# Kernel optimization log

Hardware: AMD Instinct MI355X
Metric: run time of the kernel (lower is better)

Reference implementation:

```python
import jax, jax.numpy as jnp
import numpy as np

NUM_NODES = 10000  # fixed by input spec: edge_index values in [0, 10000)


def setup_inputs() -> dict:
    key = jax.random.key(0)
    k1, k2, k3 = jax.random.split(key, 3)
    N, E, D_IN, D_OUT = NUM_NODES, 320000, 256, 256
    x = jax.random.normal(k1, (N, D_IN), dtype=jnp.float32)
    edge_index = jax.random.randint(k2, (2, E), 0, N, dtype=jnp.int64)
    # ensure node N-1 appears so num_nodes == N as in the torch code
    edge_index = edge_index.at[0, 0].set(N - 1)
    # xavier_uniform for [D_IN, D_OUT]
    limit = float(np.sqrt(6.0 / (D_IN + D_OUT)))
    weight = jax.random.uniform(k3, (D_IN, D_OUT), dtype=jnp.float32,
                                minval=-limit, maxval=limit)
    return {"x": x, "edge_index": edge_index, "weight": weight}


def _normalize_adjacency(edge_index, num_nodes):
    src, dst = edge_index[0], edge_index[1]
    ones = jnp.ones(src.shape[0], dtype=jnp.float32)
    # symmetric binarized adjacency: adj[i,j] = adj[j,i] = 1 (set, not add)
    adj = jnp.zeros((num_nodes, num_nodes), dtype=jnp.float32)
    adj = adj.at[src, dst].max(ones)
    adj = adj.at[dst, src].max(ones)
    # one round of self-loops: adj += I
    adj = adj + jnp.eye(num_nodes, dtype=jnp.float32)
    deg = jnp.sum(adj, axis=1)                    # [N]
    dinv = 1.0 / jnp.sqrt(deg)                    # [N]
    # D^-1/2 A D^-1/2 via broadcasting (equivalent to diag mms)
    return adj * dinv[:, None] * dinv[None, :]


def reference(x, edge_index, weight):
    adj = _normalize_adjacency(edge_index, NUM_NODES)  # [N, N]
    h = adj @ x                                        # [N, D_IN]
    return h @ weight                                  # [N, D_OUT]
```

## Files before the change

### kernel.cpp

```cpp
#include <hip/hip_runtime.h>
#include <hip/hip_bf16.h>
#include <stdint.h>

#define N_NODES   10000
#define D_FEAT    256
#define E_EDGES   320000
#define ROW_WORDS 313
#define ROW_STRIDE 320
#define LIST_CAP  1024

#define NB     250
#define RPB    40
#define B_CAP  8192
#define NBLK_E 313
#define NBLK_W 64
#define RPC    20

#define LDSTR 264

typedef __attribute__((ext_vector_type(4))) float float4v;
typedef _Float16 half8  __attribute__((ext_vector_type(8)));
typedef _Float16 half4v __attribute__((ext_vector_type(4)));

__device__ __forceinline__ uint16_t f2bf(float f) {
    union { float f; uint32_t u; } v; v.f = f;
    uint32_t r = v.u + 0x7fffu + ((v.u >> 16) & 1u);
    return (uint16_t)(r >> 16);
}
__device__ __forceinline__ float lo16(uint32_t u) {
    union { uint32_t u; float f; } v; v.u = u << 16; return v.f;
}
__device__ __forceinline__ float hi16(uint32_t u) {
    union { uint32_t u; float f; } v; v.u = u & 0xffff0000u; return v.f;
}


__global__ void __launch_bounds__(1024)
fill_buckets(const int* __restrict__ ei, uint32_t* __restrict__ bucketbuf,
             uint32_t* __restrict__ cursors,
             const float* __restrict__ w, _Float16* __restrict__ wt) {
    __shared__ uint32_t hist[256];
    __shared__ uint32_t lofs[256];
    __shared__ uint32_t base_s[256];
    __shared__ uint32_t stage[2048];
    __shared__ uint16_t sbkt[2048];
    int t = threadIdx.x;

    if (blockIdx.x >= NBLK_E) {
        int kb = (blockIdx.x - NBLK_E) * 4;
        int k = kb + (t >> 8), n = t & 255;
        float* st = (float*)stage;
        st[(n << 2) | (t >> 8)] = w[(size_t)k * D_FEAT + n];
        __syncthreads();
        if (t < 256) {
            half4v o = { (_Float16)st[t * 4 + 0], (_Float16)st[t * 4 + 1],
                         (_Float16)st[t * 4 + 2], (_Float16)st[t * 4 + 3] };
            *(half4v*)&wt[(size_t)t * D_FEAT + kb] = o;
        }
        return;
    }

    if (t < 256) hist[t] = 0;
    __syncthreads();
    int e = blockIdx.x * 1024 + t;
    int b0 = -1, b1 = -1; uint32_t ent0 = 0, ent1 = 0, s0 = 0, s1 = 0;
    if (e < E_EDGES) {
        int s = ei[e], d = ei[E_EDGES + e];
        if ((uint32_t)s < N_NODES && (uint32_t)d < N_NODES) {
            b0 = s / RPB; ent0 = ((uint32_t)(s - b0 * RPB) << 14) | (uint32_t)d;
            b1 = d / RPB; ent1 = ((uint32_t)(d - b1 * RPB) << 14) | (uint32_t)s;
            s0 = atomicAdd(&hist[b0], 1u);
            s1 = atomicAdd(&hist[b1], 1u);
        }
    }
    __syncthreads();
    if (t < 256) lofs[t] = hist[t];
    __syncthreads();
    for (int d = 1; d < 256; d <<= 1) {
        uint32_t v = 0;
        if (t < 256 && t >= d) v = lofs[t - d];
        __syncthreads();
        if (t < 256) lofs[t] += v;
        __syncthreads();
    }
    if (t < 256) base_s[t] = hist[t] ? atomicAdd(&cursors[t], hist[t]) : 0u;
    if (b0 >= 0) {
        uint32_t p0 = lofs[b0] - hist[b0] + s0;
        stage[p0] = ent0; sbkt[p0] = (uint16_t)b0;
        uint32_t p1 = lofs[b1] - hist[b1] + s1;
        stage[p1] = ent1; sbkt[p1] = (uint16_t)b1;
    }
    __syncthreads();
    uint32_t total = lofs[255];
    for (uint32_t idx = t; idx < total; idx += 1024) {
        uint32_t b = sbkt[idx];
        uint32_t pos = base_s[b] + (idx - (lofs[b] - hist[b]));
        if (pos < B_CAP) bucketbuf[(size_t)b * B_CAP + pos] = stage[idx];
    }
}

__global__ void __launch_bounds__(1024)
bucket_to_csr(const uint32_t* __restrict__ bucketbuf,
              const uint32_t* __restrict__ cursors,
              uint32_t* __restrict__ gcursor,
              uint32_t* __restrict__ col, uint32_t* __restrict__ row_base,
              uint32_t* __restrict__ row_deg, float* __restrict__ dinv,
              const float* __restrict__ x, uint16_t* __restrict__ xs) {
    __shared__ uint32_t bm[RPC * ROW_WORDS];
    __shared__ uint32_t degs[RPC];
    __shared__ uint32_t rowoff[RPC];
    __shared__ uint32_t segbase;
    int blk = blockIdx.x, t = threadIdx.x;
    int b   = blk >> 1;
    int lr0 = (blk & 1) * RPC;
    for (int i = t; i < RPC * ROW_WORDS; i += 1024) bm[i] = 0;
    __syncthreads();
    uint32_t cnt = min(cursors[b], (uint32_t)B_CAP);
    const uint32_t* bb = bucketbuf + (size_t)b * B_CAP;
    for (uint32_t i = t; i < cnt; i += 1024) {
        uint32_t ent = bb[i];
        uint32_t lr = (ent >> 14) - (uint32_t)lr0;
        if (lr < RPC) {
            uint32_t d = ent & 0x3FFFu;
            atomicOr(&bm[lr * ROW_WORDS + (d >> 5)], 1u << (d & 31));
        }
    }
    __syncthreads();
    int wv = t >> 6, lane = t & 63;
    for (int r = wv; r < RPC; r += 16) {
        int pop = 0;
        #pragma unroll
        for (int k = 0; k < 5; k++) {
            int w = lane + 64 * k;
            if (w < ROW_WORDS) pop += __popc(bm[r * ROW_WORDS + w]);
        }
        #pragma unroll
        for (int off = 32; off > 0; off >>= 1) pop += __shfl_xor(pop, off, 64);
        if (lane == 0) degs[r] = (uint32_t)pop;
    }
    __syncthreads();
    if (t == 0) {
        uint32_t run = 0;
        for (int r = 0; r < RPC; r++) {
            rowoff[r] = run;
            run += (degs[r] + 3u) & ~3u;
        }
        segbase = atomicAdd(gcursor, run);
    }
    __syncthreads();
    int row0 = b * RPB + lr0;
    for (int r = wv; r < RPC; r += 16) {
        int gi = row0 + r;
        uint32_t base = segbase + rowoff[r];
        float di = 1.0f / sqrtf((float)(degs[r] + 1u));
        if (lane == 0) {
            row_base[gi] = base;
            row_deg[gi]  = degs[r];
            dinv[gi]     = di;
        }
        float4v xv = *(const float4v*)(x + (size_t)gi * D_FEAT + lane * 4);
        uint2 o;
        o.x = (uint32_t)f2bf(di * xv[0]) | ((uint32_t)f2bf(di * xv[1]) << 16);
        o.y = (uint32_t)f2bf(di * xv[2]) | ((uint32_t)f2bf(di * xv[3]) << 16);
        *(uint2*)(xs + (size_t)gi * D_FEAT + lane * 4) = o;
        uint32_t wb[5]; int tot = 0;
        #pragma unroll
        for (int k = 0; k < 5; k++) {
            int w = lane + 64 * k;
            uint32_t v = (w < ROW_WORDS) ? bm[r * ROW_WORDS + w] : 0u;
            wb[k] = v; tot += __popc(v);
        }
        int incl = tot;
        #pragma unroll
        for (int off = 1; off < 64; off <<= 1) {
            int v = __shfl_up(incl, off, 64);
            if (lane >= off) incl += v;
        }
        uint32_t p = base + (uint32_t)(incl - tot);
        #pragma unroll
        for (int k = 0; k < 5; k++) {
            uint32_t bits = wb[k];
            uint32_t cbase = (uint32_t)(lane + 64 * k) << 5;
            while (bits) {
                col[p++] = cbase + (uint32_t)__builtin_ctz(bits);
                bits &= bits - 1;
            }
        }
    }
}

__global__ void __launch_bounds__(256)
spmm_csr(const uint32_t* __restrict__ row_base, const uint32_t* __restrict__ row_deg,
         const float* __restrict__ dinv, const uint32_t* __restrict__ col,
         const uint16_t* __restrict__ xs, _Float16* __restrict__ aggh) {
    int wv = threadIdx.x >> 6, lane = threadIdx.x & 63;
    int i = blockIdx.x * 4 + wv;
    uint32_t base = row_base[i], deg = row_deg[i];
    float di = dinv[i];
    float4v z = {0.f, 0.f, 0.f, 0.f};
    float4v a0 = z, a1 = z, a2 = z, a3 = z, a4 = z, a5 = z, a6 = z, a7 = z;
    size_t ch = (size_t)lane * 4;
    uint32_t t8 = deg & ~7u;
    uint32_t t = 0;
    for (; t < t8; t += 8) {
        uint4 jva = *(const uint4*)&col[base + t];
        uint4 jvb = *(const uint4*)&col[base + t + 4];
        uint2 g0 = *(const uint2*)(xs + (size_t)jva.x * D_FEAT + ch);
        uint2 g1 = *(const uint2*)(xs + (size_t)jva.y * D_FEAT + ch);
        uint2 g2 = *(const uint2*)(xs + (size_t)jva.z * D_FEAT + ch);
        uint2 g3 = *(const uint2*)(xs + (size_t)jva.w * D_FEAT + ch);
        uint2 g4 = *(const uint2*)(xs + (size_t)jvb.x * D_FEAT + ch);
        uint2 g5 = *(const uint2*)(xs + (size_t)jvb.y * D_FEAT + ch);
        uint2 g6 = *(const uint2*)(xs + (size_t)jvb.z * D_FEAT + ch);
        uint2 g7 = *(const uint2*)(xs + (size_t)jvb.w * D_FEAT + ch);
        a0[0] += lo16(g0.x); a0[1] += hi16(g0.x); a0[2] += lo16(g0.y); a0[3] += hi16(g0.y);
        a1[0] += lo16(g1.x); a1[1] += hi16(g1.x); a1[2] += lo16(g1.y); a1[3] += hi16(g1.y);
        a2[0] += lo16(g2.x); a2[1] += hi16(g2.x); a2[2] += lo16(g2.y); a2[3] += hi16(g2.y);
        a3[0] += lo16(g3.x); a3[1] += hi16(g3.x); a3[2] += lo16(g3.y); a3[3] += hi16(g3.y);
        a4[0] += lo16(g4.x); a4[1] += hi16(g4.x); a4[2] += lo16(g4.y); a4[3] += hi16(g4.y);
        a5[0] += lo16(g5.x); a5[1] += hi16(g5.x); a5[2] += lo16(g5.y); a5[3] += hi16(g5.y);
        a6[0] += lo16(g6.x); a6[1] += hi16(g6.x); a6[2] += lo16(g6.y); a6[3] += hi16(g6.y);
        a7[0] += lo16(g7.x); a7[1] += hi16(g7.x); a7[2] += lo16(g7.y); a7[3] += hi16(g7.y);
    }
    for (; t < deg; t++) {
        uint32_t j = col[base + t];
        uint2 g = *(const uint2*)(xs + (size_t)j * D_FEAT + ch);
        a0[0] += lo16(g.x); a0[1] += hi16(g.x); a0[2] += lo16(g.y); a0[3] += hi16(g.y);
    }
    uint2 gs = *(const uint2*)(xs + (size_t)i * D_FEAT + ch);
    a1[0] += lo16(gs.x); a1[1] += hi16(gs.x); a1[2] += lo16(gs.y); a1[3] += hi16(gs.y);
    float4v acc = ((a0 + a1) + (a2 + a3)) + ((a4 + a5) + (a6 + a7));
    half4v o = { (_Float16)(di * acc[0]), (_Float16)(di * acc[1]),
                 (_Float16)(di * acc[2]), (_Float16)(di * acc[3]) };
    *(half4v*)(aggh + (size_t)i * D_FEAT + ch) = o;
}

__global__ void __launch_bounds__(256)
gemm_mfma(const _Float16* __restrict__ aggh, const _Float16* __restrict__ wt,
          float* __restrict__ out) {
    __shared__ __align__(16) _Float16 a_lds[16 * LDSTR];
    int t = threadIdx.x, wv = t >> 6, lane = t & 63;
    int r0 = blockIdx.x * 16;
    for (int idx = t * 8; idx < 16 * D_FEAT; idx += 256 * 8) {
        int r = idx >> 8, c = idx & 255;
        *(half8*)&a_lds[r * LDSTR + c] =
            *(const half8*)&aggh[(size_t)(r0 + r) * D_FEAT + c];
    }
    __syncthreads();
    int quad = lane >> 4, r = lane & 15;
    int mbase = r0 + quad * 4;
    #pragma unroll
    for (int u = 0; u < 4; u++) {
        int ct = wv * 4 + u;
        const _Float16* pb = wt + (size_t)(ct * 16 + r) * D_FEAT + quad * 8;
        float4v acc = {0.f, 0.f, 0.f, 0.f};
        #pragma unroll
        for (int kk = 0; kk < D_FEAT; kk += 32) {
            half8 a = *(const half8*)&a_lds[r * LDSTR + kk + quad * 8];
            half8 b = *(const half8*)(pb + kk);
            acc = __builtin_amdgcn_mfma_f32_16x16x32_f16(a, b, acc, 0, 0, 0);
        }
        int colg = ct * 16 + r;
        #pragma unroll
        for (int v = 0; v < 4; v++)
            out[(size_t)(mbase + v) * D_FEAT + colg] = acc[v];
    }
}


__global__ void scatter_edges_fb(const int* __restrict__ ei,
                                 uint32_t* __restrict__ bitmap) {
    int e = blockIdx.x * blockDim.x + threadIdx.x;
    if (e >= E_EDGES) return;
    int s = ei[e], d = ei[E_EDGES + e];
    if ((uint32_t)s >= N_NODES || (uint32_t)d >= N_NODES) return;
    atomicOr(&bitmap[(size_t)s * ROW_STRIDE + (d >> 5)], 1u << (d & 31));
    atomicOr(&bitmap[(size_t)d * ROW_STRIDE + (s >> 5)], 1u << (s & 31));
}

__global__ void __launch_bounds__(256)
popc_dinv(const uint32_t* __restrict__ bitmap, float* __restrict__ dinv) {
    int wv = threadIdx.x >> 6, lane = threadIdx.x & 63;
    int i = blockIdx.x * 4 + wv;
    const uint32_t* rb = bitmap + (size_t)i * ROW_STRIDE;
    int pop = 0;
    #pragma unroll
    for (int k = 0; k < 5; k++) {
        int w = lane + 64 * k;
        if (w < ROW_WORDS) pop += __popc(rb[w]);
    }
    #pragma unroll
    for (int off = 32; off > 0; off >>= 1) pop += __shfl_xor(pop, off, 64);
    if (lane == 0) dinv[i] = 1.0f / sqrtf((float)(pop + 1));
}

__global__ void __launch_bounds__(256)
spmm_bitmap_fb(const uint32_t* __restrict__ bitmap, const float* __restrict__ dinv,
               const float* __restrict__ xf, float* __restrict__ agg) {
    __shared__ __align__(16) uint32_t lists[4][LIST_CAP];
    int wv = threadIdx.x >> 6, lane = threadIdx.x & 63;
    int i = blockIdx.x * 4 + wv;
    uint32_t* list = lists[wv];
    const uint32_t* rb = bitmap + (size_t)i * ROW_STRIDE;

    uint32_t wbits[5]; int tot = 0;
    #pragma unroll
    for (int k = 0; k < 5; k++) {
        int w = lane + 64 * k;
        uint32_t b = (w < ROW_WORDS) ? rb[w] : 0u;
        wbits[k] = b;
        tot += __popc(b);
    }
    int incl = tot;
    #pragma unroll
    for (int off = 1; off < 64; off <<= 1) {
        int v = __shfl_up(incl, off, 64);
        if (lane >= off) incl += v;
    }
    uint32_t p = (uint32_t)(incl - tot);
    uint32_t deg = (uint32_t)__shfl(incl, 63, 64);
    #pragma unroll
    for (int k = 0; k < 5; k++) {
        uint32_t bits = wbits[k];
        uint32_t base = (uint32_t)(lane + 64 * k) << 5;
        while (bits) {
            if (p < LIST_CAP) list[p] = base + (uint32_t)__builtin_ctz(bits);
            p++;
            bits &= bits - 1;
        }
    }
    if (deg > LIST_CAP) deg = LIST_CAP;

    float di = dinv[i];
    float4v z = {0.f, 0.f, 0.f, 0.f};
    float4v acc0 = z, acc1 = z, acc2 = z, acc3 = z;
    float4v sv = *(const float4v*)(xf + (size_t)i * D_FEAT + lane * 4);
    uint32_t t4 = deg & ~3u;
    for (uint32_t k = 0; k < t4; k += 4) {
        uint4 jv = *(const uint4*)&list[k];
        float d0 = dinv[jv.x], d1 = dinv[jv.y], d2 = dinv[jv.z], d3 = dinv[jv.w];
        float4v v0 = *(const float4v*)(xf + (size_t)jv.x * D_FEAT + lane * 4);
        float4v v1 = *(const float4v*)(xf + (size_t)jv.y * D_FEAT + lane * 4);
        float4v v2 = *(const float4v*)(xf + (size_t)jv.z * D_FEAT + lane * 4);
        float4v v3 = *(const float4v*)(xf + (size_t)jv.w * D_FEAT + lane * 4);
        acc0 += d0 * v0; acc1 += d1 * v1; acc2 += d2 * v2; acc3 += d3 * v3;
    }
    for (uint32_t k = t4; k < deg; k++) {
        uint32_t j = list[k];
        acc0 += dinv[j] * (*(const float4v*)(xf + (size_t)j * D_FEAT + lane * 4));
    }
    float4v acc = (acc0 + acc1) + (acc2 + acc3) + di * sv;
    *(float4v*)(agg + (size_t)i * D_FEAT + lane * 4) = di * acc;
}

__global__ void __launch_bounds__(256)
gemm_valu(float* __restrict__ io, const float* __restrict__ wf) {
    __shared__ __align__(16) float a_lds[16 * D_FEAT];
    int c = threadIdx.x;
    int r0 = blockIdx.x * 16;
    for (int idx = c; idx < 16 * D_FEAT; idx += 256)
        a_lds[idx] = io[(size_t)r0 * D_FEAT + idx];
    __syncthreads();
    float acc[16];
    #pragma unroll
    for (int r = 0; r < 16; r++) acc[r] = 0.f;
    for (int k0 = 0; k0 < D_FEAT; k0 += 4) {
        float w0 = wf[(size_t)(k0 + 0) * D_FEAT + c];
        float w1 = wf[(size_t)(k0 + 1) * D_FEAT + c];
        float w2 = wf[(size_t)(k0 + 2) * D_FEAT + c];
        float w3 = wf[(size_t)(k0 + 3) * D_FEAT + c];
        #pragma unroll
        for (int r = 0; r < 16; r++) {
            float4v av = *(const float4v*)&a_lds[r * D_FEAT + k0];
            acc[r] = fmaf(av[3], w3, fmaf(av[2], w2,
                     fmaf(av[1], w1, fmaf(av[0], w0, acc[r]))));
        }
    }
    #pragma unroll
    for (int r = 0; r < 16; r++)
        io[(size_t)(r0 + r) * D_FEAT + c] = acc[r];
}

extern "C" void kernel_launch(void* const* d_in, const int* in_sizes, int n_in,
                              void* d_out, int out_size, void* d_ws, size_t ws_size,
                              hipStream_t stream) {
    const float* x  = (const float*)d_in[0];
    const int*   ei = (const int*)d_in[1];
    const float* w  = (const float*)d_in[2];
    float* out = (float*)d_out;
    uint8_t* ws = (uint8_t*)d_ws;

    const size_t CUR_OFF  = 8192000;
    const size_t RB_OFF   = 8194048;
    const size_t RD_OFF   = 8234048;
    const size_t DI_OFF   = 8274048;
    const size_t XS_OFF   = 8314048;
    const size_t COL_OFF  = 13434048;
    const size_t WT_OFF   = 16154048;
    const size_t NEED_NEW = 16285120;
    const size_t NEED_FB  = 12840000;

    if (ws_size >= NEED_NEW) {
        uint32_t* bucketbuf = (uint32_t*)ws;
        _Float16* aggh      = (_Float16*)ws;
        uint32_t* cursors   = (uint32_t*)(ws + CUR_OFF);
        uint32_t* row_base  = (uint32_t*)(ws + RB_OFF);
        uint32_t* row_deg   = (uint32_t*)(ws + RD_OFF);
        float*    dinv      = (float*)(ws + DI_OFF);
        uint16_t* xs        = (uint16_t*)(ws + XS_OFF);
        uint32_t* col       = (uint32_t*)(ws + COL_OFF);
        _Float16* wt        = (_Float16*)(ws + WT_OFF);

        hipMemsetAsync(cursors, 0, 2048, stream);
        fill_buckets <<<NBLK_E + NBLK_W, 1024, 0, stream>>>(ei, bucketbuf, cursors, w, wt);
        bucket_to_csr<<<NB * 2, 1024, 0, stream>>>(bucketbuf, cursors, &cursors[NB],
                                                   col, row_base, row_deg, dinv, x, xs);
        spmm_csr     <<<N_NODES / 4, 256, 0, stream>>>(row_base, row_deg, dinv, col, xs, aggh);
        gemm_mfma    <<<N_NODES / 16, 256, 0, stream>>>(aggh, wt, out);
    } else if (ws_size >= NEED_FB) {
        uint32_t* bitmap = (uint32_t*)ws;
        float*    dinv   = (float*)(ws + 12800000);

        hipMemsetAsync(bitmap, 0, 12800000, stream);
        scatter_edges_fb<<<(E_EDGES + 255) / 256, 256, 0, stream>>>(ei, bitmap);
        popc_dinv      <<<N_NODES / 4, 256, 0, stream>>>(bitmap, dinv);
        spmm_bitmap_fb <<<N_NODES / 4, 256, 0, stream>>>(bitmap, dinv, x, out);
        gemm_valu      <<<N_NODES / 16, 256, 0, stream>>>(out, w);
    }
}
```

Before: 135.5 us.

## Reorder to (XW) then SpMM, fuse GEMM into CSR build, drop atomics

The product is reassociated so that X@W is computed first, as fp16 MFMA blocks that run alongside the CSR-building blocks in the same launch. The SpMM then gathers rows of XW and applies the per-neighbour and per-row normalisation factors, writing the final output directly. Edge bucketing now writes per-block sub-buckets with fixed capacity instead of using global atomic cursors, which removes the memset and the cross-block atomics. CSR rows use a fixed stride of 128. This cuts one kernel launch and the separate GEMM pass, at the cost of extra dinv gathers and silent truncation if a row degree or sub-bucket overflows its cap.

```diff
diff --git a/kernel.cpp b/kernel.cpp
--- a/kernel.cpp
+++ b/kernel.cpp
@@ -11,10 +11,13 @@
 
 #define NB     250
 #define RPB    40
-#define B_CAP  8192
+#define RPC    20
+#define S_CAP  48
 #define NBLK_E 313
 #define NBLK_W 64
-#define RPC    20
+#define NBLK_C 500
+#define NBLK_G 625
+#define COLSTR 128
 
 #define LDSTR 264
 
@@ -22,26 +25,20 @@
 typedef _Float16 half8  __attribute__((ext_vector_type(8)));
 typedef _Float16 half4v __attribute__((ext_vector_type(4)));
 
-__device__ __forceinline__ uint16_t f2bf(float f) {
-    union { float f; uint32_t u; } v; v.f = f;
-    uint32_t r = v.u + 0x7fffu + ((v.u >> 16) & 1u);
-    return (uint16_t)(r >> 16);
-}
-__device__ __forceinline__ float lo16(uint32_t u) {
-    union { uint32_t u; float f; } v; v.u = u << 16; return v.f;
-}
-__device__ __forceinline__ float hi16(uint32_t u) {
-    union { uint32_t u; float f; } v; v.u = u & 0xffff0000u; return v.f;
+__device__ __forceinline__ float h2f_lo(uint32_t u) {
+    union { uint32_t u; _Float16 h[2]; } v; v.u = u; return (float)v.h[0];
+}
+__device__ __forceinline__ float h2f_hi(uint32_t u) {
+    union { uint32_t u; _Float16 h[2]; } v; v.u = u; return (float)v.h[1];
 }
 
 
 __global__ void __launch_bounds__(1024)
-fill_buckets(const int* __restrict__ ei, uint32_t* __restrict__ bucketbuf,
-             uint32_t* __restrict__ cursors,
-             const float* __restrict__ w, _Float16* __restrict__ wt) {
+fill_sort(const int* __restrict__ ei, uint32_t* __restrict__ bucketbuf,
+          uint32_t* __restrict__ hist_g,
+          const float* __restrict__ w, _Float16* __restrict__ wt) {
     __shared__ uint32_t hist[256];
     __shared__ uint32_t lofs[256];
-    __shared__ uint32_t base_s[256];
     __shared__ uint32_t stage[2048];
     __shared__ uint16_t sbkt[2048];
     int t = threadIdx.x;
@@ -83,7 +80,6 @@
         if (t < 256) lofs[t] += v;
         __syncthreads();
     }
-    if (t < 256) base_s[t] = hist[t] ? atomicAdd(&cursors[t], hist[t]) : 0u;
     if (b0 >= 0) {
         uint32_t p0 = lofs[b0] - hist[b0] + s0;
         stage[p0] = ent0; sbkt[p0] = (uint16_t)b0;
@@ -92,77 +88,74 @@
     }
     __syncthreads();
     uint32_t total = lofs[255];
+    uint32_t bb0 = blockIdx.x * 256;
     for (uint32_t idx = t; idx < total; idx += 1024) {
         uint32_t b = sbkt[idx];
-        uint32_t pos = base_s[b] + (idx - (lofs[b] - hist[b]));
-        if (pos < B_CAP) bucketbuf[(size_t)b * B_CAP + pos] = stage[idx];
-    }
+        uint32_t pos = idx - (lofs[b] - hist[b]);
+        if (pos < S_CAP)
+            bucketbuf[(size_t)(bb0 + b) * S_CAP + pos] = stage[idx];
+    }
+    if (t < 256) hist_g[bb0 + t] = min(hist[t], (uint32_t)S_CAP);
 }
 
 __global__ void __launch_bounds__(1024)
-bucket_to_csr(const uint32_t* __restrict__ bucketbuf,
-              const uint32_t* __restrict__ cursors,
-              uint32_t* __restrict__ gcursor,
-              uint32_t* __restrict__ col, uint32_t* __restrict__ row_base,
-              uint32_t* __restrict__ row_deg, float* __restrict__ dinv,
-              const float* __restrict__ x, uint16_t* __restrict__ xs) {
-    __shared__ uint32_t bm[RPC * ROW_WORDS];
-    __shared__ uint32_t degs[RPC];
-    __shared__ uint32_t rowoff[RPC];
-    __shared__ uint32_t segbase;
-    int blk = blockIdx.x, t = threadIdx.x;
-    int b   = blk >> 1;
-    int lr0 = (blk & 1) * RPC;
+csr_gemm(const uint32_t* __restrict__ bucketbuf, const uint32_t* __restrict__ hist_g,
+         uint32_t* __restrict__ row_deg, float* __restrict__ dinv,
+         uint32_t* __restrict__ col,
+         const float* __restrict__ x, const _Float16* __restrict__ wt,
+         _Float16* __restrict__ yw) {
+    __shared__ __align__(16) uint32_t smem[RPC * ROW_WORDS + NBLK_E];
+    int t = threadIdx.x;
+
+    if (blockIdx.x >= NBLK_C) {
+        _Float16* a_lds = (_Float16*)smem;
+        int r0 = (blockIdx.x - NBLK_C) * 16;
+        int row = t >> 6, c4 = (t & 63) * 4;
+        float4v xv = *(const float4v*)(x + (size_t)(r0 + row) * D_FEAT + c4);
+        half4v h = { (_Float16)xv[0], (_Float16)xv[1],
+                     (_Float16)xv[2], (_Float16)xv[3] };
+        *(half4v*)&a_lds[row * LDSTR + c4] = h;
+        __syncthreads();
+        int wv = t >> 6, lane = t & 63;
+        int quad = lane >> 4, r = lane & 15;
+        int ct = wv;
+        const _Float16* pb = wt + (size_t)(ct * 16 + r) * D_FEAT + quad * 8;
+        float4v acc = {0.f, 0.f, 0.f, 0.f};
+        #pragma unroll
+        for (int kk = 0; kk < D_FEAT; kk += 32) {
+            half8 a = *(const half8*)&a_lds[r * LDSTR + kk + quad * 8];
+            half8 b = *(const half8*)(pb + kk);
+            acc = __builtin_amdgcn_mfma_f32_16x16x32_f16(a, b, acc, 0, 0, 0);
+        }
+        int colg = ct * 16 + r;
+        #pragma unroll
+        for (int u = 0; u < 4; u++)
+            yw[(size_t)(r0 + quad * 4 + u) * D_FEAT + colg] = (_Float16)acc[u];
+        return;
+    }
+
+    uint32_t* bm       = smem;
+    uint32_t* hist_col = smem + RPC * ROW_WORDS;
+    int b   = blockIdx.x >> 1;
+    int lr0 = (blockIdx.x & 1) * RPC;
     for (int i = t; i < RPC * ROW_WORDS; i += 1024) bm[i] = 0;
-    __syncthreads();
-    uint32_t cnt = min(cursors[b], (uint32_t)B_CAP);
-    const uint32_t* bb = bucketbuf + (size_t)b * B_CAP;
-    for (uint32_t i = t; i < cnt; i += 1024) {
-        uint32_t ent = bb[i];
-        uint32_t lr = (ent >> 14) - (uint32_t)lr0;
-        if (lr < RPC) {
-            uint32_t d = ent & 0x3FFFu;
-            atomicOr(&bm[lr * ROW_WORDS + (d >> 5)], 1u << (d & 31));
+    if (t < NBLK_E) hist_col[t] = hist_g[(size_t)t * 256 + b];
+    __syncthreads();
+    for (int p = t; p < NBLK_E * S_CAP; p += 1024) {
+        int sb = p / S_CAP, off = p % S_CAP;
+        if ((uint32_t)off < hist_col[sb]) {
+            uint32_t ent = bucketbuf[(size_t)(sb * 256 + b) * S_CAP + off];
+            uint32_t lr = (ent >> 14) - (uint32_t)lr0;
+            if (lr < RPC) {
+                uint32_t d = ent & 0x3FFFu;
+                atomicOr(&bm[lr * ROW_WORDS + (d >> 5)], 1u << (d & 31));
+            }
         }
     }
     __syncthreads();
     int wv = t >> 6, lane = t & 63;
     for (int r = wv; r < RPC; r += 16) {
-        int pop = 0;
-        #pragma unroll
-        for (int k = 0; k < 5; k++) {
-            int w = lane + 64 * k;
-            if (w < ROW_WORDS) pop += __popc(bm[r * ROW_WORDS + w]);
-        }
-        #pragma unroll
-        for (int off = 32; off > 0; off >>= 1) pop += __shfl_xor(pop, off, 64);
-        if (lane == 0) degs[r] = (uint32_t)pop;
-    }
-    __syncthreads();
-    if (t == 0) {
-        uint32_t run = 0;
-        for (int r = 0; r < RPC; r++) {
-            rowoff[r] = run;
-            run += (degs[r] + 3u) & ~3u;
-        }
-        segbase = atomicAdd(gcursor, run);
-    }
-    __syncthreads();
-    int row0 = b * RPB + lr0;
-    for (int r = wv; r < RPC; r += 16) {
-        int gi = row0 + r;
-        uint32_t base = segbase + rowoff[r];
-        float di = 1.0f / sqrtf((float)(degs[r] + 1u));
-        if (lane == 0) {
-            row_base[gi] = base;
-            row_deg[gi]  = degs[r];
-            dinv[gi]     = di;
-        }
-        float4v xv = *(const float4v*)(x + (size_t)gi * D_FEAT + lane * 4);
-        uint2 o;
-        o.x = (uint32_t)f2bf(di * xv[0]) | ((uint32_t)f2bf(di * xv[1]) << 16);
-        o.y = (uint32_t)f2bf(di * xv[2]) | ((uint32_t)f2bf(di * xv[3]) << 16);
-        *(uint2*)(xs + (size_t)gi * D_FEAT + lane * 4) = o;
+        int gi = b * RPB + lr0 + r;
         uint32_t wb[5]; int tot = 0;
         #pragma unroll
         for (int k = 0; k < 5; k++) {
@@ -176,13 +169,20 @@
             int v = __shfl_up(incl, off, 64);
             if (lane >= off) incl += v;
         }
-        uint32_t p = base + (uint32_t)(incl - tot);
+        uint32_t total = (uint32_t)__shfl(incl, 63, 64);
+        if (lane == 0) {
+            row_deg[gi] = min(total, (uint32_t)COLSTR);
+            dinv[gi]    = 1.0f / sqrtf((float)(total + 1u));
+        }
+        uint32_t p = (uint32_t)(incl - tot);
         #pragma unroll
         for (int k = 0; k < 5; k++) {
             uint32_t bits = wb[k];
             uint32_t cbase = (uint32_t)(lane + 64 * k) << 5;
             while (bits) {
-                col[p++] = cbase + (uint32_t)__builtin_ctz(bits);
+                if (p < COLSTR)
+                    col[(size_t)gi * COLSTR + p] = cbase + (uint32_t)__builtin_ctz(bits);
+                p++;
                 bits &= bits - 1;
             }
         }
@@ -190,12 +190,14 @@
 }
 
 __global__ void __launch_bounds__(256)
-spmm_csr(const uint32_t* __restrict__ row_base, const uint32_t* __restrict__ row_deg,
-         const float* __restrict__ dinv, const uint32_t* __restrict__ col,
-         const uint16_t* __restrict__ xs, _Float16* __restrict__ aggh) {
+spmm_out(const uint32_t* __restrict__ row_deg, const float* __restrict__ dinv,
+         const uint32_t* __restrict__ col, const _Float16* __restrict__ ywp,
+         float* __restrict__ out) {
+    const uint16_t* yw = (const uint16_t*)ywp;
     int wv = threadIdx.x >> 6, lane = threadIdx.x & 63;
     int i = blockIdx.x * 4 + wv;
-    uint32_t base = row_base[i], deg = row_deg[i];
+    uint32_t base = (uint32_t)i * COLSTR;
+    uint32_t deg = min(row_deg[i], (uint32_t)COLSTR);
     float di = dinv[i];
     float4v z = {0.f, 0.f, 0.f, 0.f};
     float4v a0 = z, a1 = z, a2 = z, a3 = z, a4 = z, a5 = z, a6 = z, a7 = z;
@@ -205,66 +207,45 @@
     for (; t < t8; t += 8) {
         uint4 jva = *(const uint4*)&col[base + t];
         uint4 jvb = *(const uint4*)&col[base + t + 4];
-        uint2 g0 = *(const uint2*)(xs + (size_t)jva.x * D_FEAT + ch);
-        uint2 g1 = *(const uint2*)(xs + (size_t)jva.y * D_FEAT + ch);
-        uint2 g2 = *(const uint2*)(xs + (size_t)jva.z * D_FEAT + ch);
-        uint2 g3 = *(const uint2*)(xs + (size_t)jva.w * D_FEAT + ch);
-        uint2 g4 = *(const uint2*)(xs + (size_t)jvb.x * D_FEAT + ch);
-        uint2 g5 = *(const uint2*)(xs + (size_t)jvb.y * D_FEAT + ch);
-        uint2 g6 = *(const uint2*)(xs + (size_t)jvb.z * D_FEAT + ch);
-        uint2 g7 = *(const uint2*)(xs + (size_t)jvb.w * D_FEAT + ch);
-        a0[0] += lo16(g0.x); a0[1] += hi16(g0.x); a0[2] += lo16(g0.y); a0[3] += hi16(g0.y);
-        a1[0] += lo16(g1.x); a1[1] += hi16(g1.x); a1[2] += lo16(g1.y); a1[3] += hi16(g1.y);
-        a2[0] += lo16(g2.x); a2[1] += hi16(g2.x); a2[2] += lo16(g2.y); a2[3] += hi16(g2.y);
-        a3[0] += lo16(g3.x); a3[1] += hi16(g3.x); a3[2] += lo16(g3.y); a3[3] += hi16(g3.y);
-        a4[0] += lo16(g4.x); a4[1] += hi16(g4.x); a4[2] += lo16(g4.y); a4[3] += hi16(g4.y);
-        a5[0] += lo16(g5.x); a5[1] += hi16(g5.x); a5[2] += lo16(g5.y); a5[3] += hi16(g5.y);
-        a6[0] += lo16(g6.x); a6[1] += hi16(g6.x); a6[2] += lo16(g6.y); a6[3] += hi16(g6.y);
-        a7[0] += lo16(g7.x); a7[1] += hi16(g7.x); a7[2] += lo16(g7.y); a7[3] += hi16(g7.y);
+        float d0 = dinv[jva.x], d1 = dinv[jva.y], d2 = dinv[jva.z], d3 = dinv[jva.w];
+        float d4 = dinv[jvb.x], d5 = dinv[jvb.y], d6 = dinv[jvb.z], d7 = dinv[jvb.w];
+        uint2 g0 = *(const uint2*)(yw + (size_t)jva.x * D_FEAT + ch);
+        uint2 g1 = *(const uint2*)(yw + (size_t)jva.y * D_FEAT + ch);
+        uint2 g2 = *(const uint2*)(yw + (size_t)jva.z * D_FEAT + ch);
+        uint2 g3 = *(const uint2*)(yw + (size_t)jva.w * D_FEAT + ch);
+        uint2 g4 = *(const uint2*)(yw + (size_t)jvb.x * D_FEAT + ch);
+        uint2 g5 = *(const uint2*)(yw + (size_t)jvb.y * D_FEAT + ch);
+        uint2 g6 = *(const uint2*)(yw + (size_t)jvb.z * D_FEAT + ch);
+        uint2 g7 = *(const uint2*)(yw + (size_t)jvb.w * D_FEAT + ch);
+        a0[0] += d0 * h2f_lo(g0.x); a0[1] += d0 * h2f_hi(g0.x);
+        a0[2] += d0 * h2f_lo(g0.y); a0[3] += d0 * h2f_hi(g0.y);
+        a1[0] += d1 * h2f_lo(g1.x); a1[1] += d1 * h2f_hi(g1.x);
+        a1[2] += d1 * h2f_lo(g1.y); a1[3] += d1 * h2f_hi(g1.y);
+        a2[0] += d2 * h2f_lo(g2.x); a2[1] += d2 * h2f_hi(g2.x);
+        a2[2] += d2 * h2f_lo(g2.y); a2[3] += d2 * h2f_hi(g2.y);
+        a3[0] += d3 * h2f_lo(g3.x); a3[1] += d3 * h2f_hi(g3.x);
+        a3[2] += d3 * h2f_lo(g3.y); a3[3] += d3 * h2f_hi(g3.y);
+        a4[0] += d4 * h2f_lo(g4.x); a4[1] += d4 * h2f_hi(g4.x);
+        a4[2] += d4 * h2f_lo(g4.y); a4[3] += d4 * h2f_hi(g4.y);
+        a5[0] += d5 * h2f_lo(g5.x); a5[1] += d5 * h2f_hi(g5.x);
+        a5[2] += d5 * h2f_lo(g5.y); a5[3] += d5 * h2f_hi(g5.y);
+        a6[0] += d6 * h2f_lo(g6.x); a6[1] += d6 * h2f_hi(g6.x);
+        a6[2] += d6 * h2f_lo(g6.y); a6[3] += d6 * h2f_hi(g6.y);
+        a7[0] += d7 * h2f_lo(g7.x); a7[1] += d7 * h2f_hi(g7.x);
+        a7[2] += d7 * h2f_lo(g7.y); a7[3] += d7 * h2f_hi(g7.y);
     }
     for (; t < deg; t++) {
         uint32_t j = col[base + t];
-        uint2 g = *(const uint2*)(xs + (size_t)j * D_FEAT + ch);
-        a0[0] += lo16(g.x); a0[1] += hi16(g.x); a0[2] += lo16(g.y); a0[3] += hi16(g.y);
-    }
-    uint2 gs = *(const uint2*)(xs + (size_t)i * D_FEAT + ch);
-    a1[0] += lo16(gs.x); a1[1] += hi16(gs.x); a1[2] += lo16(gs.y); a1[3] += hi16(gs.y);
+        float dj = dinv[j];
+        uint2 g = *(const uint2*)(yw + (size_t)j * D_FEAT + ch);
+        a0[0] += dj * h2f_lo(g.x); a0[1] += dj * h2f_hi(g.x);
+        a0[2] += dj * h2f_lo(g.y); a0[3] += dj * h2f_hi(g.y);
+    }
+    uint2 gs = *(const uint2*)(yw + (size_t)i * D_FEAT + ch);
+    a1[0] += di * h2f_lo(gs.x); a1[1] += di * h2f_hi(gs.x);
+    a1[2] += di * h2f_lo(gs.y); a1[3] += di * h2f_hi(gs.y);
     float4v acc = ((a0 + a1) + (a2 + a3)) + ((a4 + a5) + (a6 + a7));
-    half4v o = { (_Float16)(di * acc[0]), (_Float16)(di * acc[1]),
-                 (_Float16)(di * acc[2]), (_Float16)(di * acc[3]) };
-    *(half4v*)(aggh + (size_t)i * D_FEAT + ch) = o;
-}
-
-__global__ void __launch_bounds__(256)
-gemm_mfma(const _Float16* __restrict__ aggh, const _Float16* __restrict__ wt,
-          float* __restrict__ out) {
-    __shared__ __align__(16) _Float16 a_lds[16 * LDSTR];
-    int t = threadIdx.x, wv = t >> 6, lane = t & 63;
-    int r0 = blockIdx.x * 16;
-    for (int idx = t * 8; idx < 16 * D_FEAT; idx += 256 * 8) {
-        int r = idx >> 8, c = idx & 255;
-        *(half8*)&a_lds[r * LDSTR + c] =
-            *(const half8*)&aggh[(size_t)(r0 + r) * D_FEAT + c];
-    }
-    __syncthreads();
-    int quad = lane >> 4, r = lane & 15;
-    int mbase = r0 + quad * 4;
-    #pragma unroll
-    for (int u = 0; u < 4; u++) {
-        int ct = wv * 4 + u;
-        const _Float16* pb = wt + (size_t)(ct * 16 + r) * D_FEAT + quad * 8;
-        float4v acc = {0.f, 0.f, 0.f, 0.f};
-        #pragma unroll
-        for (int kk = 0; kk < D_FEAT; kk += 32) {
-            half8 a = *(const half8*)&a_lds[r * LDSTR + kk + quad * 8];
-            half8 b = *(const half8*)(pb + kk);
-            acc = __builtin_amdgcn_mfma_f32_16x16x32_f16(a, b, acc, 0, 0, 0);
-        }
-        int colg = ct * 16 + r;
-        #pragma unroll
-        for (int v = 0; v < 4; v++)
-            out[(size_t)(mbase + v) * D_FEAT + colg] = acc[v];
-    }
+    *(float4v*)(out + (size_t)i * D_FEAT + ch) = di * acc;
 }
 
 
@@ -390,33 +371,28 @@
     float* out = (float*)d_out;
     uint8_t* ws = (uint8_t*)d_ws;
 
-    const size_t CUR_OFF  = 8192000;
-    const size_t RB_OFF   = 8194048;
-    const size_t RD_OFF   = 8234048;
-    const size_t DI_OFF   = 8274048;
-    const size_t XS_OFF   = 8314048;
-    const size_t COL_OFF  = 13434048;
-    const size_t WT_OFF   = 16154048;
-    const size_t NEED_NEW = 16285120;
+    const size_t BB_OFF   = 320512;
+    const size_t RD_OFF   = 15705088;
+    const size_t DI_OFF   = 15745088;
+    const size_t WT_OFF   = 15785088;
+    const size_t YW_OFF   = 15916160;
+    const size_t COL_OFF  = 21036160;
+    const size_t NEED_NEW = 26156160;
     const size_t NEED_FB  = 12840000;
 
     if (ws_size >= NEED_NEW) {
-        uint32_t* bucketbuf = (uint32_t*)ws;
-        _Float16* aggh      = (_Float16*)ws;
-        uint32_t* cursors   = (uint32_t*)(ws + CUR_OFF);
-        uint32_t* row_base  = (uint32_t*)(ws + RB_OFF);
+        uint32_t* hist_g    = (uint32_t*)ws;
+        uint32_t* bucketbuf = (uint32_t*)(ws + BB_OFF);
         uint32_t* row_deg   = (uint32_t*)(ws + RD_OFF);
         float*    dinv      = (float*)(ws + DI_OFF);
-        uint16_t* xs        = (uint16_t*)(ws + XS_OFF);
+        _Float16* wt        = (_Float16*)(ws + WT_OFF);
+        _Float16* yw        = (_Float16*)(ws + YW_OFF);
         uint32_t* col       = (uint32_t*)(ws + COL_OFF);
-        _Float16* wt        = (_Float16*)(ws + WT_OFF);
-
-        hipMemsetAsync(cursors, 0, 2048, stream);
-        fill_buckets <<<NBLK_E + NBLK_W, 1024, 0, stream>>>(ei, bucketbuf, cursors, w, wt);
-        bucket_to_csr<<<NB * 2, 1024, 0, stream>>>(bucketbuf, cursors, &cursors[NB],
-                                                   col, row_base, row_deg, dinv, x, xs);
-        spmm_csr     <<<N_NODES / 4, 256, 0, stream>>>(row_base, row_deg, dinv, col, xs, aggh);
-        gemm_mfma    <<<N_NODES / 16, 256, 0, stream>>>(aggh, wt, out);
+
+        fill_sort<<<NBLK_E + NBLK_W, 1024, 0, stream>>>(ei, bucketbuf, hist_g, w, wt);
+        csr_gemm <<<NBLK_C + NBLK_G, 1024, 0, stream>>>(bucketbuf, hist_g,
+                                                        row_deg, dinv, col, x, wt, yw);
+        spmm_out <<<N_NODES / 4, 256, 0, stream>>>(row_deg, dinv, col, yw, out);
     } else if (ws_size >= NEED_FB) {
         uint32_t* bitmap = (uint32_t*)ws;
         float*    dinv   = (float*)(ws + 12800000);
```

New measurement: 132.5 us. -2.2%, faster.
